# Kernel optimization log

Measured on AMD Instinct MI355X. Metric: run time of the kernel, lower is better.

The kernel has to match this reference:

```python
import jax, jax.numpy as jnp
import numpy as np

N_EL = 4            # allowed elements (H, C, N, O)
N_EXPERTS = N_EL * N_EL
F_ATOM = 176        # per-atom symmetry feature dim
F_PAIR = 32         # pair feature dim (2*F_ATOM + F_PAIR == 384 == nodes[0])


def _init_linear(key, fin, fout, n):
    # torch nn.Linear default init: U(-1/sqrt(fin), 1/sqrt(fin))
    bound = 1.0 / np.sqrt(fin)
    kw, kb = jax.random.split(key)
    W = jax.random.uniform(kw, (n, fin, fout), minval=-bound, maxval=bound, dtype=jnp.float32)
    b = jax.random.uniform(kb, (n, fout), minval=-bound, maxval=bound, dtype=jnp.float32)
    return W, b


def setup_inputs() -> dict:
    key = jax.random.key(0)
    ks = jax.random.split(key, 8)
    B, A, C = 128, 128, 256
    elements = jax.random.randint(ks[0], (B, A), 0, N_EL)
    connectivity = jax.random.randint(ks[1], (B, C, 2), 0, A)
    sym_features = jax.random.normal(ks[2], (B, A, F_ATOM), dtype=jnp.float32)
    pair_features = jax.random.normal(ks[3], (B, C, F_PAIR), dtype=jnp.float32)
    W1, b1 = _init_linear(ks[4], 384, 128, N_EXPERTS)
    W2, b2 = _init_linear(ks[5], 128, 96, N_EXPERTS)
    W3, b3 = _init_linear(ks[6], 96, 2, N_EXPERTS)
    return dict(elements=elements, connectivity=connectivity,
                sym_features=sym_features, pair_features=pair_features,
                W1=W1, b1=b1, W2=W2, b2=b2, W3=W3, b3=b3)


def _pair_moe(elements, connectivity, sym_features, pair_features, W1, b1, W2, b2, W3, b3):
    B, C, _ = connectivity.shape
    A = sym_features.shape[1]
    out_dim = W3.shape[-1]

    # mirror: mask padded pairs (connectivity[...,0] == -1) before offsetting
    mask = (connectivity[..., 0] != -1).reshape(-1)              # [B*C]
    conn_f = (connectivity + (jnp.arange(B) * A)[:, None, None]).reshape(-1, 2)
    idx0 = jnp.where(mask, conn_f[:, 0], 0)
    idx1 = jnp.where(mask, conn_f[:, 1], 0)

    feat_f = sym_features.reshape(-1, sym_features.shape[-1])    # [B*A, F]
    el_f = elements.reshape(-1)                                  # [B*A]

    m = mask[:, None].astype(sym_features.dtype)
    fa = feat_f[idx0] * m                                        # [B*C, F] (zeros where padded)
    fb = feat_f[idx1] * m
    e0 = jnp.where(mask, el_f[idx0], -1)
    e1 = jnp.where(mask, el_f[idx1], -1)
    nn_index = e0 * N_EL + e1                                    # -5 for padded pairs -> no expert

    x = jnp.concatenate([fa, fb, pair_features.reshape(-1, pair_features.shape[-1])], axis=1)

    y = jnp.zeros((x.shape[0], out_dim), dtype=x.dtype)
    for i in range(N_EXPERTS):  # fixed small expert set (structural loop)
        h = jax.nn.celu(x @ W1[i] + b1[i])
        h = jax.nn.celu(h @ W2[i] + b2[i])
        o = h @ W3[i] + b3[i]
        y = jnp.where((nn_index == i)[:, None], o, y)
    return y.reshape(B, C, out_dim)


def reference(elements, connectivity, sym_features, pair_features, W1, b1, W2, b2, W3, b3):
    # Original returns (elements, connectivity, y); only y is computed output.
    return _pair_moe(elements, connectivity, sym_features, pair_features, W1, b1, W2, b2, W3, b3)
```

## Files before the change

kernel.cpp:

```cpp
#include <hip/hip_runtime.h>
#include <math.h>

typedef __attribute__((ext_vector_type(8))) short short8;
typedef __attribute__((ext_vector_type(4))) float f32x4;

namespace {
constexpr int NEL   = 4;
constexpr int NEXP  = 16;
constexpr int Bb    = 128;
constexpr int Aa    = 128;
constexpr int Cc    = 256;
constexpr int FATOM = 176;
constexpr int FPAIR = 32;
constexpr int FIN   = 384;
constexpr int HH1   = 128;
constexpr int HH2   = 96;
constexpr int NP    = Bb * Cc;
constexpr int BUCKET_CAP = 4096;

constexpr int WS_COUNTS = 0;
constexpr int WS_BUCKET = 64;

constexpr int W2_OFF = 12 * HH1 * 32;
constexpr int WPK_E  = W2_OFF + 4 * HH2 * 32;
}

__device__ inline short f2bf(float f) {
    unsigned u = __builtin_bit_cast(unsigned, f);
    unsigned r = (u + 0x7FFFu + ((u >> 16) & 1u)) >> 16;
    return (short)r;
}
__device__ inline float celu1(float v) {
    return v > 0.f ? v : (__expf(v) - 1.0f);
}
__device__ inline short8 cvt8(const float* p) {
    float4 lo = *(const float4*)p;
    float4 hi = *(const float4*)(p + 4);
    short8 r;
    r[0] = f2bf(lo.x); r[1] = f2bf(lo.y); r[2] = f2bf(lo.z); r[3] = f2bf(lo.w);
    r[4] = f2bf(hi.x); r[5] = f2bf(hi.y); r[6] = f2bf(hi.z); r[7] = f2bf(hi.w);
    return r;
}

__global__ __launch_bounds__(256) void k_idx(
    const int* __restrict__ conn, const int* __restrict__ elements,
    int* __restrict__ counts, int* __restrict__ bucket,
    float* __restrict__ out)
{
    __shared__ int sh_cnt[NEXP], sh_base[NEXP];
    int t = threadIdx.x;
    int p = blockIdx.x * 256 + t;
    if (t < NEXP) sh_cnt[t] = 0;
    __syncthreads();
    int e = -1, r = 0;
    {
        int c0 = conn[2 * p], c1 = conn[2 * p + 1];
        if (c0 != -1) {
            int b = p / Cc;
            int i0 = b * Aa + c0; if (i0 < 0) i0 += Bb * Aa;
            int i1 = b * Aa + c1; if (i1 < 0) i1 += Bb * Aa;
            e = elements[i0] * NEL + elements[i1];
        }
        if (e < 0 || e >= NEXP) {
            out[2 * p] = 0.f; out[2 * p + 1] = 0.f;
            e = -1;
        } else {
            r = atomicAdd(&sh_cnt[e], 1);
        }
    }
    __syncthreads();
    if (t < NEXP) sh_base[t] = (sh_cnt[t] > 0) ? atomicAdd(&counts[t], sh_cnt[t]) : 0;
    __syncthreads();
    if (e >= 0) {
        int pos = sh_base[e] + r;
        if (pos < BUCKET_CAP) bucket[e * BUCKET_CAP + pos] = p;
    }
}

__global__ __launch_bounds__(512, 2) void k_moe(
    const int* __restrict__ counts, const int* __restrict__ bucket,
    const int* __restrict__ conn,
    const float* __restrict__ sym, const float* __restrict__ pairf,
    const float* __restrict__ W1, const float* __restrict__ W2,
    const float* __restrict__ b1, const float* __restrict__ b2,
    const float* __restrict__ W3, const float* __restrict__ b3,
    float* __restrict__ out)
{
    __shared__ short Wlds[WPK_E];
    __shared__ short H1s[8][16 * HH1];

    int e     = blockIdx.x & 15;
    int shard = blockIdx.x >> 4;
    int cnt = counts[e];
    if (cnt > BUCKET_CAP) cnt = BUCKET_CAP;

    int t = threadIdx.x;
    int w = t >> 6;
    int lane = t & 63;
    int lr = lane & 15, lg = (lane >> 4) & 3;

    {
        const float* W1e = W1 + (size_t)e * FIN * HH1;
#pragma unroll
        for (int rr = 0; rr < 3; ++rr) {
            int s = t + 512 * rr;
            int ks = s >> 7, n = s & 127;
            const float* src = W1e + (size_t)(ks * 32) * HH1 + n;
#pragma unroll
            for (int q = 0; q < 4; ++q) {
                short8 v;
#pragma unroll
                for (int j = 0; j < 8; ++j)
                    v[j] = f2bf(src[(size_t)(q * 8 + j) * HH1]);
                *(short8*)&Wlds[(ks * HH1 + n) * 32 + 8 * q] = v;
            }
        }
        if (t < 384) {
            int q4 = t / 96, n2 = t % 96;
            const float* src = W2 + (size_t)e * HH1 * HH2 + (size_t)(q4 * 32) * HH2 + n2;
#pragma unroll
            for (int q = 0; q < 4; ++q) {
                short8 v;
#pragma unroll
                for (int j = 0; j < 8; ++j)
                    v[j] = f2bf(src[(size_t)(q * 8 + j) * HH2]);
                *(short8*)&Wlds[W2_OFF + (q4 * HH2 + n2) * 32 + 8 * q] = v;
            }
        }
    }

    float b1v[8];
#pragma unroll
    for (int j = 0; j < 8; ++j) b1v[j] = b1[e * HH1 + j * 16 + lr];
    float2 b3v = ((const float2*)b3)[e];

    __syncthreads();

    int nt = (cnt + 15) >> 4;
    const int* bucket_e = bucket + e * BUCKET_CAP;
    short* h1w = &H1s[w][0];

    for (int tile = shard * 8 + w; tile < nt; tile += 128) {
        int ii = tile * 16 + lr;
        int p = bucket_e[ii < cnt ? ii : cnt - 1];
        int2 c = ((const int2*)conn)[p];
        int bb = (p >> 8) << 7;
        const float* fa = sym + (size_t)(bb + c.x) * FATOM;
        const float* fb = sym + (size_t)(bb + c.y) * FATOM;
        const float* pf = pairf + (size_t)p * FPAIR;

        short8 a[12];
        a[0]  = cvt8(fa + 8 * lg);
        a[1]  = cvt8(fa + 32 + 8 * lg);
        a[2]  = cvt8(fa + 64 + 8 * lg);
        a[3]  = cvt8(fa + 96 + 8 * lg);
        a[4]  = cvt8(fa + 128 + 8 * lg);
        a[5]  = cvt8((lg < 2 ? fa + 160 : fb - 16) + 8 * lg);
        a[6]  = cvt8(fb + 16 + 8 * lg);
        a[7]  = cvt8(fb + 48 + 8 * lg);
        a[8]  = cvt8(fb + 80 + 8 * lg);
        a[9]  = cvt8(fb + 112 + 8 * lg);
        a[10] = cvt8(fb + 144 + 8 * lg);
        a[11] = cvt8(pf + 8 * lg);

        f32x4 acc[8];
#pragma unroll
        for (int j = 0; j < 8; ++j) acc[j] = (f32x4){b1v[j], b1v[j], b1v[j], b1v[j]};
#pragma unroll
        for (int ks = 0; ks < 12; ++ks) {
#pragma unroll
            for (int j = 0; j < 8; ++j) {
                short8 bw = *(const short8*)&Wlds[(ks * HH1 + j * 16 + lr) * 32 + 8 * lg];
                acc[j] = __builtin_amdgcn_mfma_f32_16x16x32_bf16(a[ks], bw, acc[j], 0, 0, 0);
            }
        }

#pragma unroll
        for (int j = 0; j < 8; ++j)
#pragma unroll
            for (int r2 = 0; r2 < 4; ++r2) {
                int m = 4 * lg + r2;
                int n = 16 * j + lr;
                h1w[m * HH1 + (((n >> 3) ^ (m & 7)) << 3) + (n & 7)] = f2bf(celu1(acc[j][r2]));
            }
        asm volatile("s_waitcnt lgkmcnt(0)" ::: "memory");
        __builtin_amdgcn_sched_barrier(0);

        int mx = lr & 7;
        short8 bh[4];
#pragma unroll
        for (int q = 0; q < 4; ++q)
            bh[q] = *(const short8*)&h1w[lr * HH1 + (((q * 4 + lg) ^ mx) << 3)];

        float s0 = 0.f, s1 = 0.f;
#pragma unroll
        for (int t6 = 0; t6 < 6; ++t6) {
            int n2b = 16 * t6 + 4 * lg;
            float4 bb4 = *(const float4*)&b2[e * HH2 + n2b];
            f32x4 a2;
            a2[0] = bb4.x; a2[1] = bb4.y; a2[2] = bb4.z; a2[3] = bb4.w;
#pragma unroll
            for (int q = 0; q < 4; ++q) {
                short8 aw = *(const short8*)&Wlds[W2_OFF + (q * HH2 + 16 * t6 + lr) * 32 + 8 * lg];
                a2 = __builtin_amdgcn_mfma_f32_16x16x32_bf16(aw, bh[q], a2, 0, 0, 0);
            }
            float4 w3a = *(const float4*)&W3[(size_t)(e * HH2 + n2b) * 2];
            float4 w3b = *(const float4*)&W3[(size_t)(e * HH2 + n2b) * 2 + 4];
            float h0 = celu1(a2[0]), h1 = celu1(a2[1]), h2 = celu1(a2[2]), h3 = celu1(a2[3]);
            s0 = fmaf(h0, w3a.x, fmaf(h1, w3a.z, fmaf(h2, w3b.x, fmaf(h3, w3b.z, s0))));
            s1 = fmaf(h0, w3a.y, fmaf(h1, w3a.w, fmaf(h2, w3b.y, fmaf(h3, w3b.w, s1))));
        }
        s0 += __shfl_xor(s0, 16); s0 += __shfl_xor(s0, 32);
        s1 += __shfl_xor(s1, 16); s1 += __shfl_xor(s1, 32);
        if (((lane >> 4) & 3) == 0 && ii < cnt) {
            float2 o2; o2.x = s0 + b3v.x; o2.y = s1 + b3v.y;
            *(float2*)(out + 2 * (size_t)bucket_e[ii]) = o2;
        }
    }
}

extern "C" void kernel_launch(void* const* d_in, const int* in_sizes, int n_in,
                              void* d_out, int out_size, void* d_ws, size_t ws_size,
                              hipStream_t stream)
{
    const int*   elements = (const int*)d_in[0];
    const int*   conn     = (const int*)d_in[1];
    const float* sym      = (const float*)d_in[2];
    const float* pairf    = (const float*)d_in[3];
    const float* W1       = (const float*)d_in[4];
    const float* b1       = (const float*)d_in[5];
    const float* W2       = (const float*)d_in[6];
    const float* b2       = (const float*)d_in[7];
    const float* W3       = (const float*)d_in[8];
    const float* b3       = (const float*)d_in[9];
    float* out = (float*)d_out;

    int* wsi    = (int*)d_ws;
    int* counts = wsi + WS_COUNTS;
    int* bucket = wsi + WS_BUCKET;

    hipMemsetAsync((void*)counts, 0, NEXP * sizeof(int), stream);

    k_idx<<<NP / 256, 256, 0, stream>>>(conn, elements, counts, bucket, out);
    k_moe<<<256, 512, 0, stream>>>(counts, bucket, conn, sym, pairf,
                                   W1, W2, b1, b2, W3, b3, out);
}
```

Baseline: 38.49 us.

## Prepack bf16 weights in prep kernel and prefetch first tile before weight barrier

Weight transposition and bf16 conversion move out of each MoE block into a prep kernel that shares a launch with the bucketing work, writing a packed layout to the workspace. Each MoE block then copies its expert's packed weights with contiguous vector loads instead of 16 blocks per expert doing strided scalar conversion. The first tile's gather is issued before the LDS store and barrier so its latency overlaps the weight load. The cost is an extra global write and read of the packed weights and higher register pressure from holding 15 vectors plus the prefetched tile.

```diff
diff --git a/kernel.cpp b/kernel.cpp
--- a/kernel.cpp
+++ b/kernel.cpp
@@ -20,9 +20,17 @@
 
 constexpr int WS_COUNTS = 0;
 constexpr int WS_BUCKET = 64;
+constexpr int WS_WPK    = 65600;
 
 constexpr int W2_OFF = 12 * HH1 * 32;
 constexpr int WPK_E  = W2_OFF + 4 * HH2 * 32;
+
+constexpr int W1_BLOCKS  = 768;
+constexpr int W2_BLOCKS  = 192;
+constexpr int IDX_BLOCKS = NP / 256;
+constexpr int W2_BASE  = W1_BLOCKS;
+constexpr int IDX_BASE = W1_BLOCKS + W2_BLOCKS;
+constexpr int PREP_GRID = IDX_BASE + IDX_BLOCKS;
 }
 
 __device__ inline short f2bf(float f) {
@@ -42,38 +50,73 @@
     return r;
 }
 
-__global__ __launch_bounds__(256) void k_idx(
+__global__ __launch_bounds__(256) void k_prep(
+    const float* __restrict__ W1, const float* __restrict__ W2,
+    short* __restrict__ wpk,
     const int* __restrict__ conn, const int* __restrict__ elements,
     int* __restrict__ counts, int* __restrict__ bucket,
     float* __restrict__ out)
 {
+    __shared__ float T[32][33];
     __shared__ int sh_cnt[NEXP], sh_base[NEXP];
+
+    int bid = blockIdx.x;
     int t = threadIdx.x;
-    int p = blockIdx.x * 256 + t;
-    if (t < NEXP) sh_cnt[t] = 0;
-    __syncthreads();
-    int e = -1, r = 0;
-    {
-        int c0 = conn[2 * p], c1 = conn[2 * p + 1];
-        if (c0 != -1) {
-            int b = p / Cc;
-            int i0 = b * Aa + c0; if (i0 < 0) i0 += Bb * Aa;
-            int i1 = b * Aa + c1; if (i1 < 0) i1 += Bb * Aa;
-            e = elements[i0] * NEL + elements[i1];
-        }
-        if (e < 0 || e >= NEXP) {
-            out[2 * p] = 0.f; out[2 * p + 1] = 0.f;
-            e = -1;
+
+    if (bid < IDX_BASE) {
+        const float* src; short* dst; int N, k0, n0;
+        if (bid < W2_BASE) {
+            int e = bid / 48, tl = bid % 48;
+            N = HH1; k0 = (tl % 12) * 32; n0 = (tl / 12) * 32;
+            src = W1 + (size_t)e * FIN * HH1;
+            dst = wpk + (size_t)e * WPK_E;
         } else {
-            r = atomicAdd(&sh_cnt[e], 1);
-        }
-    }
-    __syncthreads();
-    if (t < NEXP) sh_base[t] = (sh_cnt[t] > 0) ? atomicAdd(&counts[t], sh_cnt[t]) : 0;
-    __syncthreads();
-    if (e >= 0) {
-        int pos = sh_base[e] + r;
-        if (pos < BUCKET_CAP) bucket[e * BUCKET_CAP + pos] = p;
+            int b2i = bid - W2_BASE;
+            int e = b2i / 12, tl = b2i % 12;
+            N = HH2; k0 = (tl % 4) * 32; n0 = (tl / 4) * 32;
+            src = W2 + (size_t)e * HH1 * HH2;
+            dst = wpk + (size_t)e * WPK_E + W2_OFF;
+        }
+        int tx = t & 31, ty = t >> 5;
+        int ks = k0 >> 5;
+#pragma unroll
+        for (int j = 0; j < 4; ++j) {
+            int r = ty + 8 * j;
+            T[r][tx] = src[(size_t)(k0 + r) * N + n0 + tx];
+        }
+        __syncthreads();
+#pragma unroll
+        for (int j = 0; j < 4; ++j) {
+            int n = n0 + ty + 8 * j;
+            dst[(size_t)(ks * N + n) * 32 + tx] = f2bf(T[tx][ty + 8 * j]);
+        }
+    } else {
+        int p = (bid - IDX_BASE) * 256 + t;
+        if (t < NEXP) sh_cnt[t] = 0;
+        __syncthreads();
+        int e = -1, r = 0;
+        {
+            int c0 = conn[2 * p], c1 = conn[2 * p + 1];
+            if (c0 != -1) {
+                int b = p / Cc;
+                int i0 = b * Aa + c0; if (i0 < 0) i0 += Bb * Aa;
+                int i1 = b * Aa + c1; if (i1 < 0) i1 += Bb * Aa;
+                e = elements[i0] * NEL + elements[i1];
+            }
+            if (e < 0 || e >= NEXP) {
+                out[2 * p] = 0.f; out[2 * p + 1] = 0.f;
+                e = -1;
+            } else {
+                r = atomicAdd(&sh_cnt[e], 1);
+            }
+        }
+        __syncthreads();
+        if (t < NEXP) sh_base[t] = (sh_cnt[t] > 0) ? atomicAdd(&counts[t], sh_cnt[t]) : 0;
+        __syncthreads();
+        if (e >= 0) {
+            int pos = sh_base[e] + r;
+            if (pos < BUCKET_CAP) bucket[e * BUCKET_CAP + pos] = p;
+        }
     }
 }
 
@@ -81,7 +124,7 @@
     const int* __restrict__ counts, const int* __restrict__ bucket,
     const int* __restrict__ conn,
     const float* __restrict__ sym, const float* __restrict__ pairf,
-    const float* __restrict__ W1, const float* __restrict__ W2,
+    const short* __restrict__ wpk,
     const float* __restrict__ b1, const float* __restrict__ b2,
     const float* __restrict__ W3, const float* __restrict__ b3,
     float* __restrict__ out)
@@ -93,76 +136,58 @@
     int shard = blockIdx.x >> 4;
     int cnt = counts[e];
     if (cnt > BUCKET_CAP) cnt = BUCKET_CAP;
+    int nt = (cnt + 15) >> 4;
 
     int t = threadIdx.x;
     int w = t >> 6;
     int lane = t & 63;
     int lr = lane & 15, lg = (lane >> 4) & 3;
 
-    {
-        const float* W1e = W1 + (size_t)e * FIN * HH1;
-#pragma unroll
-        for (int rr = 0; rr < 3; ++rr) {
-            int s = t + 512 * rr;
-            int ks = s >> 7, n = s & 127;
-            const float* src = W1e + (size_t)(ks * 32) * HH1 + n;
-#pragma unroll
-            for (int q = 0; q < 4; ++q) {
-                short8 v;
-#pragma unroll
-                for (int j = 0; j < 8; ++j)
-                    v[j] = f2bf(src[(size_t)(q * 8 + j) * HH1]);
-                *(short8*)&Wlds[(ks * HH1 + n) * 32 + 8 * q] = v;
-            }
-        }
-        if (t < 384) {
-            int q4 = t / 96, n2 = t % 96;
-            const float* src = W2 + (size_t)e * HH1 * HH2 + (size_t)(q4 * 32) * HH2 + n2;
-#pragma unroll
-            for (int q = 0; q < 4; ++q) {
-                short8 v;
-#pragma unroll
-                for (int j = 0; j < 8; ++j)
-                    v[j] = f2bf(src[(size_t)(q * 8 + j) * HH2]);
-                *(short8*)&Wlds[W2_OFF + (q4 * HH2 + n2) * 32 + 8 * q] = v;
-            }
-        }
-    }
+    const int* bucket_e = bucket + e * BUCKET_CAP;
+    const short* wsrc = wpk + (size_t)e * WPK_E;
+
+    short8 v[15];
+#pragma unroll
+    for (int r = 0; r < 15; ++r) v[r] = *(const short8*)(wsrc + r * 4096 + t * 8);
+
+    int tile0 = shard * 8 + w;
+    int ii0 = tile0 * 16 + lr;
+    int idx0 = (tile0 < nt) ? (ii0 < cnt ? ii0 : (cnt > 0 ? cnt - 1 : 0)) : 0;
+    int p0 = bucket_e[idx0] & (NP - 1);
+    int2 c0 = ((const int2*)conn)[p0];
 
     float b1v[8];
 #pragma unroll
     for (int j = 0; j < 8; ++j) b1v[j] = b1[e * HH1 + j * 16 + lr];
     float2 b3v = ((const float2*)b3)[e];
 
+    short8 a0[12];
+    {
+        int bb = (p0 >> 8) << 7;
+        const float* fa = sym + (size_t)(bb + (c0.x & 127)) * FATOM;
+        const float* fb = sym + (size_t)(bb + (c0.y & 127)) * FATOM;
+        const float* pf = pairf + (size_t)p0 * FPAIR;
+        a0[0]  = cvt8(fa + 8 * lg);
+        a0[1]  = cvt8(fa + 32 + 8 * lg);
+        a0[2]  = cvt8(fa + 64 + 8 * lg);
+        a0[3]  = cvt8(fa + 96 + 8 * lg);
+        a0[4]  = cvt8(fa + 128 + 8 * lg);
+        a0[5]  = cvt8((lg < 2 ? fa + 160 : fb - 16) + 8 * lg);
+        a0[6]  = cvt8(fb + 16 + 8 * lg);
+        a0[7]  = cvt8(fb + 48 + 8 * lg);
+        a0[8]  = cvt8(fb + 80 + 8 * lg);
+        a0[9]  = cvt8(fb + 112 + 8 * lg);
+        a0[10] = cvt8(fb + 144 + 8 * lg);
+        a0[11] = cvt8(pf + 8 * lg);
+    }
+
+#pragma unroll
+    for (int r = 0; r < 15; ++r) *(short8*)&Wlds[r * 4096 + t * 8] = v[r];
     __syncthreads();
 
-    int nt = (cnt + 15) >> 4;
-    const int* bucket_e = bucket + e * BUCKET_CAP;
     short* h1w = &H1s[w][0];
 
-    for (int tile = shard * 8 + w; tile < nt; tile += 128) {
-        int ii = tile * 16 + lr;
-        int p = bucket_e[ii < cnt ? ii : cnt - 1];
-        int2 c = ((const int2*)conn)[p];
-        int bb = (p >> 8) << 7;
-        const float* fa = sym + (size_t)(bb + c.x) * FATOM;
-        const float* fb = sym + (size_t)(bb + c.y) * FATOM;
-        const float* pf = pairf + (size_t)p * FPAIR;
-
-        short8 a[12];
-        a[0]  = cvt8(fa + 8 * lg);
-        a[1]  = cvt8(fa + 32 + 8 * lg);
-        a[2]  = cvt8(fa + 64 + 8 * lg);
-        a[3]  = cvt8(fa + 96 + 8 * lg);
-        a[4]  = cvt8(fa + 128 + 8 * lg);
-        a[5]  = cvt8((lg < 2 ? fa + 160 : fb - 16) + 8 * lg);
-        a[6]  = cvt8(fb + 16 + 8 * lg);
-        a[7]  = cvt8(fb + 48 + 8 * lg);
-        a[8]  = cvt8(fb + 80 + 8 * lg);
-        a[9]  = cvt8(fb + 112 + 8 * lg);
-        a[10] = cvt8(fb + 144 + 8 * lg);
-        a[11] = cvt8(pf + 8 * lg);
-
+    auto do_tile = [&](const short8* a, int ii) {
         f32x4 acc[8];
 #pragma unroll
         for (int j = 0; j < 8; ++j) acc[j] = (f32x4){b1v[j], b1v[j], b1v[j], b1v[j]};
@@ -174,7 +199,6 @@
                 acc[j] = __builtin_amdgcn_mfma_f32_16x16x32_bf16(a[ks], bw, acc[j], 0, 0, 0);
             }
         }
-
 #pragma unroll
         for (int j = 0; j < 8; ++j)
 #pragma unroll
@@ -215,6 +239,33 @@
         if (((lane >> 4) & 3) == 0 && ii < cnt) {
             float2 o2; o2.x = s0 + b3v.x; o2.y = s1 + b3v.y;
             *(float2*)(out + 2 * (size_t)bucket_e[ii]) = o2;
+        }
+    };
+
+    if (tile0 < nt) {
+        do_tile(a0, ii0);
+        for (int tile = tile0 + 128; tile < nt; tile += 128) {
+            int ii = tile * 16 + lr;
+            int p = bucket_e[ii < cnt ? ii : cnt - 1] & (NP - 1);
+            int2 c = ((const int2*)conn)[p];
+            int bb = (p >> 8) << 7;
+            const float* fa = sym + (size_t)(bb + (c.x & 127)) * FATOM;
+            const float* fb = sym + (size_t)(bb + (c.y & 127)) * FATOM;
+            const float* pf = pairf + (size_t)p * FPAIR;
+            short8 a[12];
+            a[0]  = cvt8(fa + 8 * lg);
+            a[1]  = cvt8(fa + 32 + 8 * lg);
+            a[2]  = cvt8(fa + 64 + 8 * lg);
+            a[3]  = cvt8(fa + 96 + 8 * lg);
+            a[4]  = cvt8(fa + 128 + 8 * lg);
+            a[5]  = cvt8((lg < 2 ? fa + 160 : fb - 16) + 8 * lg);
+            a[6]  = cvt8(fb + 16 + 8 * lg);
+            a[7]  = cvt8(fb + 48 + 8 * lg);
+            a[8]  = cvt8(fb + 80 + 8 * lg);
+            a[9]  = cvt8(fb + 112 + 8 * lg);
+            a[10] = cvt8(fb + 144 + 8 * lg);
+            a[11] = cvt8(pf + 8 * lg);
+            do_tile(a, ii);
         }
     }
 }
@@ -238,10 +289,12 @@
     int* wsi    = (int*)d_ws;
     int* counts = wsi + WS_COUNTS;
     int* bucket = wsi + WS_BUCKET;
+    short* wpk  = (short*)(wsi + WS_WPK);
 
     hipMemsetAsync((void*)counts, 0, NEXP * sizeof(int), stream);
 
-    k_idx<<<NP / 256, 256, 0, stream>>>(conn, elements, counts, bucket, out);
-    k_moe<<<256, 512, 0, stream>>>(counts, bucket, conn, sym, pairf,
-                                   W1, W2, b1, b2, W3, b3, out);
-}
+    k_prep<<<PREP_GRID, 256, 0, stream>>>(W1, W2, wpk, conn, elements,
+                                          counts, bucket, out);
+    k_moe<<<256, 512, 0, stream>>>(counts, bucket, conn, sym, pairf, wpk,
+                                   b1, b2, W3, b3, out);
+}
```

Result: faster. 35.31 us (-8.3%).
